# Performance work log

Measured on AMD Instinct MI355X. Metric: run time of the kernel, lower is better.

## Reference

```python
import jax, jax.numpy as jnp
import numpy as np

B, S, D = 4, 2048, 128


def setup_inputs() -> dict:
    key = jax.random.key(0)
    kq, kk, kv = jax.random.split(key, 3)
    query = jax.random.normal(kq, (B, S, D), dtype=jnp.float32)
    key_t = jax.random.normal(kk, (B, S, D), dtype=jnp.float32)
    value = jax.random.normal(kv, (B, S, D), dtype=jnp.float32)
    return {"query": query, "key": key_t, "value": value}


def reference(query, key, value):
    # Raw dot-general attention: contract only the last dim, NO batch dims,
    # so scores have shape [B, Sq, B, Sk] (cross-batch attention).
    scores = jnp.einsum('aqd,bkd->aqbk', query, key)  # [B,S,B,S]
    # softmax over the trailing half of the dims (axes 2 and 3 jointly)
    attn = jax.nn.softmax(scores, axis=(2, 3))
    # Dropout: train=False -> deterministic no-op.
    # Second dot_general contracts trailing (B,Sk) of attn with leading (B,Sk) of value.
    y = jnp.einsum('aqbk,bkd->aqd', attn, value)  # [B,S,D]
    return y
```

## Files before the change

### kernel.cpp

```cpp
#include <hip/hip_runtime.h>
#include <hip/hip_bf16.h>
#include <string.h>

#define NROWS 8192
#define DH    128
#define G     8
#define KPG   (NROWS / G)
#define NIT   (KPG / 64)
#define B32U  (16 * 512)
#define LOG2E 1.44269504088896340736f
#define MSCALED (56.0f * LOG2E)

typedef __attribute__((ext_vector_type(8)))  short    short8;
typedef __attribute__((ext_vector_type(16))) float    floatx16;
typedef __attribute__((ext_vector_type(4)))  unsigned short us4;
typedef __attribute__((ext_vector_type(8)))  _Float16 half8;

#define MFMA_BF32(a, b, c)  __builtin_amdgcn_mfma_f32_32x32x16_bf16((a), (b), (c), 0, 0, 0)
#define MFMA_F16W(a, b, c)  __builtin_amdgcn_mfma_f32_32x32x16_f16((a), (b), (c), 0, 0, 0)

__device__ __forceinline__ unsigned short f32_to_bf16(float f) {
    union { float f; unsigned u; } v; v.f = f;
    unsigned u = v.u + 0x7FFFu + ((v.u >> 16) & 1u);
    return (unsigned short)(u >> 16);
}
__device__ __forceinline__ float bf16_to_f32(unsigned short h) {
    union { unsigned u; float f; } v; v.u = ((unsigned)h) << 16;
    return v.f;
}
__device__ __forceinline__ float fast_exp2(float x) {
    float r; asm("v_exp_f32 %0, %1" : "=v"(r) : "v"(x)); return r;
}
__device__ __forceinline__ void async_ld16(const void* g, void* lds) {
    __builtin_amdgcn_global_load_lds(
        (const __attribute__((address_space(1))) unsigned int*)g,
        (__attribute__((address_space(3))) unsigned int*)lds, 16, 0, 0);
}

__global__ void prep_kernel(const float* __restrict__ K, const float* __restrict__ V,
                            unsigned short* __restrict__ KV) {
    int bid = blockIdx.x;
    if (bid < 128) {
        int B = bid;
        const float* Ksrc = K + (size_t)B * 64 * DH;
        unsigned short* dst = KV + (size_t)(2 * B) * B32U;
#pragma unroll
        for (int j = 0; j < 4; j++) {
            int ch = j * 256 + threadIdx.x;
            int mt = ch >> 9;
            int rem = ch & 511;
            int c = rem >> 6;
            int within = rem & 63;
            int h = within >> 5, l31 = within & 31;
            const float* src = Ksrc + (size_t)(mt * 32 + l31) * DH + c * 16 + h * 8;
            float4 a = *(const float4*)src;
            float4 b = *(const float4*)(src + 4);
            half8 o = {(_Float16)a.x, (_Float16)a.y, (_Float16)a.z, (_Float16)a.w,
                       (_Float16)b.x, (_Float16)b.y, (_Float16)b.z, (_Float16)b.w};
            *(half8*)(dst + (size_t)mt * B32U + c * 512 + within * 8) = o;
        }
        return;
    }
    int B = bid - 128;
    __shared__ unsigned short tile[64][132];
    const float* Vsrc = V + (size_t)B * 64 * DH;
    {
        int row = threadIdx.x >> 2;
        int cb0 = (threadIdx.x & 3) * 32;
#pragma unroll
        for (int j = 0; j < 8; j++) {
            float4 v = *(const float4*)(Vsrc + (size_t)row * DH + cb0 + j * 4);
            tile[row][cb0 + j * 4 + 0] = f32_to_bf16(v.x);
            tile[row][cb0 + j * 4 + 1] = f32_to_bf16(v.y);
            tile[row][cb0 + j * 4 + 2] = f32_to_bf16(v.z);
            tile[row][cb0 + j * 4 + 3] = f32_to_bf16(v.w);
        }
    }
    __syncthreads();
    unsigned short* dstv = KV + (size_t)(2 * B) * B32U + 8 * 512;
#pragma unroll
    for (int j = 0; j < 4; j++) {
        int ch = j * 256 + threadIdx.x;
        int mt = ch >> 9;
        int rem = ch & 511;
        int seg = rem >> 6;
        int within = rem & 63;
        int h = within >> 5, rr = within & 31;
        int t = seg >> 1, sp = seg & 1;
        int d = t * 32 + rr;
        short8 o;
#pragma unroll
        for (int jj = 0; jj < 8; jj++) {
            int p = mt * 32 + sp * 16 + h * 8 + jj;
            int ar = (p & ~12) | ((p & 8) >> 1) | ((p & 4) << 1);
            o[jj] = tile[ar][d];
        }
        *(short8*)(dstv + (size_t)mt * B32U + seg * 512 + within * 8) = o;
    }
}

__launch_bounds__(256, 2)
__global__ void attn_kernel(const float* __restrict__ Q,
                            const unsigned short* __restrict__ KV,
                            unsigned short* __restrict__ Opart,
                            float* __restrict__ lsum) {
    __shared__ __align__(16) unsigned short kbuf[2][16 * 512];

    const int lane = threadIdx.x & 63;
    const int wave = threadIdx.x >> 6;
    const int g    = blockIdx.x & (G - 1);
    const int qt   = blockIdx.x >> 3;
    const int l31  = lane & 31;
    const int h    = lane >> 5;
    const int qrow0 = qt * 128 + wave * 32;

    half8 qf[8];
    {
        const float* qs = Q + (size_t)(qrow0 + l31) * DH + h * 8;
#pragma unroll
        for (int c = 0; c < 8; c++) {
            float4 a = *(const float4*)(qs + c * 16);
            float4 b = *(const float4*)(qs + c * 16 + 4);
            qf[c] = half8{(_Float16)a.x, (_Float16)a.y, (_Float16)a.z, (_Float16)a.w,
                          (_Float16)b.x, (_Float16)b.y, (_Float16)b.z, (_Float16)b.w};
        }
    }

    floatx16 Oacc[4];
#pragma unroll
    for (int t = 0; t < 4; t++)
#pragma unroll
        for (int e = 0; e < 16; e++) Oacc[t][e] = 0.f;
    float lacc = 0.f;

    const unsigned short* pk = KV + (size_t)(g * (KPG / 32)) * B32U + lane * 8;
    const unsigned short* pv = KV + (size_t)(g * (KPG / 32)) * B32U + 8 * 512 + lane * 8;
    auto stage = [&](int buf) {
        unsigned short* dst = kbuf[buf];
#pragma unroll
        for (int j = 0; j < 4; j++) {
            int s = wave + 4 * j;
            int mt = s >> 3, c = s & 7;
            async_ld16(pk + (size_t)(mt * 16 + c) * 512, dst + s * 512);
        }
        pk += 2 * B32U;
    };

    const int fo = lane * 8;

    stage(0);
    for (int it = 0; it < NIT; ++it) {
        __syncthreads();

        short8 vf[16];
#pragma unroll
        for (int s = 0; s < 16; s++) {
            int mt = s >> 3, ss = s & 7;
            vf[s] = *(const short8*)(pv + (size_t)mt * B32U + ss * 512);
        }
        pv += 2 * B32U;

        if (it + 1 < NIT) stage((it + 1) & 1);

        const unsigned short* cb = kbuf[it & 1];

        floatx16 S0, S1;
#pragma unroll
        for (int e = 0; e < 16; e++) { S0[e] = 0.f; S1[e] = 0.f; }
        __builtin_amdgcn_s_setprio(1);
#pragma unroll
        for (int c = 0; c < 8; c++) {
            half8 a0 = *(const half8*)(cb + c * 512 + fo);
            half8 a1 = *(const half8*)(cb + (8 + c) * 512 + fo);
            S0 = MFMA_F16W(a0, qf[c], S0);
            S1 = MFMA_F16W(a1, qf[c], S1);
        }
        __builtin_amdgcn_s_setprio(0);

        short8 bp0[2], bp1[2];
        auto expack = [&](const floatx16& S, short8 (&bp)[2]) {
#pragma unroll
            for (int sp = 0; sp < 2; sp++) {
                union { unsigned u[4]; short8 s8; } pkk;
                float l0 = 0.f, l1 = 0.f;
#pragma unroll
                for (int e = 0; e < 4; e++) {
                    float pa  = fast_exp2(__builtin_fmaf(S[8 * sp + 2 * e],     LOG2E, -MSCALED));
                    float pb2 = fast_exp2(__builtin_fmaf(S[8 * sp + 2 * e + 1], LOG2E, -MSCALED));
                    l0 += pa; l1 += pb2;
                    __hip_bfloat162 c2 = __float22bfloat162_rn(float2{pa, pb2});
                    unsigned u; memcpy(&u, &c2, 4);
                    pkk.u[e] = u;
                }
                lacc += l0 + l1;
                bp[sp] = pkk.s8;
            }
        };
        expack(S0, bp0);
        expack(S1, bp1);

        __builtin_amdgcn_s_setprio(1);
#pragma unroll
        for (int t = 0; t < 4; t++) {
            Oacc[t] = MFMA_BF32(vf[2 * t],     bp0[0], Oacc[t]);
            Oacc[t] = MFMA_BF32(vf[8 + 2 * t], bp1[0], Oacc[t]);
        }
#pragma unroll
        for (int t = 0; t < 4; t++) {
            Oacc[t] = MFMA_BF32(vf[2 * t + 1], bp0[1], Oacc[t]);
            Oacc[t] = MFMA_BF32(vf[9 + 2 * t], bp1[1], Oacc[t]);
        }
        __builtin_amdgcn_s_setprio(0);
    }

    unsigned short* op = Opart + ((size_t)g * NROWS + qrow0 + l31) * DH;
#pragma unroll
    for (int t = 0; t < 4; t++)
#pragma unroll
        for (int rg = 0; rg < 4; rg++) {
            us4 w;
#pragma unroll
            for (int e = 0; e < 4; e++) w[e] = f32_to_bf16(Oacc[t][4 * rg + e]);
            *(us4*)(op + 32 * t + 8 * rg + 4 * h) = w;
        }
    lacc += __shfl_xor(lacc, 32);
    if (h == 0) lsum[(size_t)g * NROWS + qrow0 + l31] = lacc;
}

__global__ void merge_kernel(const unsigned short* __restrict__ Opart,
                             const float* __restrict__ lsum, float* __restrict__ out) {
    int t = blockIdx.x * 256 + threadIdx.x;
    int base = t * 8;
    int q = base >> 7;
    float L = 0.f;
#pragma unroll
    for (int g = 0; g < G; g++) L += lsum[(size_t)g * NROWS + q];
    float acc[8] = {0.f, 0.f, 0.f, 0.f, 0.f, 0.f, 0.f, 0.f};
#pragma unroll
    for (int g = 0; g < G; g++) {
        short8 v = *(const short8*)(Opart + (size_t)g * NROWS * DH + base);
#pragma unroll
        for (int j = 0; j < 8; j++) acc[j] += bf16_to_f32((unsigned short)v[j]);
    }
    float inv = 1.0f / L;
    float4 o0 = {acc[0] * inv, acc[1] * inv, acc[2] * inv, acc[3] * inv};
    float4 o1 = {acc[4] * inv, acc[5] * inv, acc[6] * inv, acc[7] * inv};
    *(float4*)(out + base) = o0;
    *(float4*)(out + base + 4) = o1;
}

extern "C" void kernel_launch(void* const* d_in, const int* in_sizes, int n_in,
                              void* d_out, int out_size, void* d_ws, size_t ws_size,
                              hipStream_t stream) {
    const float* Q = (const float*)d_in[0];
    const float* K = (const float*)d_in[1];
    const float* V = (const float*)d_in[2];
    float* out = (float*)d_out;

    char* ws = (char*)d_ws;
    unsigned short* KV = (unsigned short*)ws;
    char* p = ws + (size_t)(NROWS / 32) * B32U * 2;
    unsigned short* Opart = (unsigned short*)p;
    float* lsum = (float*)(p + (size_t)G * NROWS * DH * sizeof(unsigned short));

    hipLaunchKernelGGL(prep_kernel, dim3(256), dim3(256), 0, stream, K, V, KV);
    hipLaunchKernelGGL(attn_kernel, dim3((NROWS / 128) * G), dim3(256), 0, stream,
                       Q, KV, Opart, lsum);
    hipLaunchKernelGGL(merge_kernel, dim3(NROWS * DH / (256 * 8)), dim3(256), 0, stream,
                       Opart, lsum, out);
}
```

Before: 120.1 us.

## Software-pipeline QK and PV MFMAs with triple-buffered K and LDS-staged V

Restructures the main loop so the QK^T scores for the next tile are computed while the PV MFMAs for the current tile run, interleaving the two MFMA streams. K is triple-buffered in LDS and V is now staged asynchronously into double-buffered LDS instead of being loaded directly from global memory into registers each iteration. This is meant to hide exp latency and global V load latency behind matrix work. In exchange it uses more LDS (five 16 KB buffers), which may reduce occupancy below two blocks per CU, and the prologue/epilogue logic becomes more complex.

```diff
diff --git a/kernel.cpp b/kernel.cpp
--- a/kernel.cpp
+++ b/kernel.cpp
@@ -104,7 +104,8 @@
                             const unsigned short* __restrict__ KV,
                             unsigned short* __restrict__ Opart,
                             float* __restrict__ lsum) {
-    __shared__ __align__(16) unsigned short kbuf[2][16 * 512];
+    __shared__ __align__(16) unsigned short kbuf[3][16 * 512];
+    __shared__ __align__(16) unsigned short vbuf[2][16 * 512];
 
     const int lane = threadIdx.x & 63;
     const int wave = threadIdx.x >> 6;
@@ -133,84 +134,117 @@
         for (int e = 0; e < 16; e++) Oacc[t][e] = 0.f;
     float lacc = 0.f;
 
-    const unsigned short* pk = KV + (size_t)(g * (KPG / 32)) * B32U + lane * 8;
-    const unsigned short* pv = KV + (size_t)(g * (KPG / 32)) * B32U + 8 * 512 + lane * 8;
-    auto stage = [&](int buf) {
-        unsigned short* dst = kbuf[buf];
+    const unsigned short* base = KV + (size_t)(g * (KPG / 32)) * B32U + lane * 8;
+    auto stageK = [&](int tt, int slot) {
+        const unsigned short* src = base + (size_t)(2 * tt) * B32U;
+        unsigned short* dst = kbuf[slot];
 #pragma unroll
         for (int j = 0; j < 4; j++) {
             int s = wave + 4 * j;
             int mt = s >> 3, c = s & 7;
-            async_ld16(pk + (size_t)(mt * 16 + c) * 512, dst + s * 512);
-        }
-        pk += 2 * B32U;
+            async_ld16(src + (size_t)mt * B32U + c * 512, dst + s * 512);
+        }
     };
+    auto stageV = [&](int tt, int slot) {
+        const unsigned short* src = base + (size_t)(2 * tt) * B32U;
+        unsigned short* dst = vbuf[slot];
+#pragma unroll
+        for (int j = 0; j < 4; j++) {
+            int s = wave + 4 * j;
+            int mt = s >> 3, sv = s & 7;
+            async_ld16(src + (size_t)mt * B32U + (8 + sv) * 512, dst + s * 512);
+        }
+    };
 
     const int fo = lane * 8;
 
-    stage(0);
-    for (int it = 0; it < NIT; ++it) {
-        __syncthreads();
-
-        short8 vf[16];
-#pragma unroll
-        for (int s = 0; s < 16; s++) {
-            int mt = s >> 3, ss = s & 7;
-            vf[s] = *(const short8*)(pv + (size_t)mt * B32U + ss * 512);
-        }
-        pv += 2 * B32U;
-
-        if (it + 1 < NIT) stage((it + 1) & 1);
-
-        const unsigned short* cb = kbuf[it & 1];
-
-        floatx16 S0, S1;
-#pragma unroll
-        for (int e = 0; e < 16; e++) { S0[e] = 0.f; S1[e] = 0.f; }
+    stageK(0, 0);
+    stageV(0, 0);
+    stageK(1, 1);
+    __syncthreads();
+
+    floatx16 S0, S1;
+#pragma unroll
+    for (int e = 0; e < 16; e++) { S0[e] = 0.f; S1[e] = 0.f; }
+    {
+        const unsigned short* kb = kbuf[0];
         __builtin_amdgcn_s_setprio(1);
 #pragma unroll
         for (int c = 0; c < 8; c++) {
-            half8 a0 = *(const half8*)(cb + c * 512 + fo);
-            half8 a1 = *(const half8*)(cb + (8 + c) * 512 + fo);
+            half8 a0 = *(const half8*)(kb + c * 512 + fo);
+            half8 a1 = *(const half8*)(kb + (8 + c) * 512 + fo);
             S0 = MFMA_F16W(a0, qf[c], S0);
             S1 = MFMA_F16W(a1, qf[c], S1);
         }
         __builtin_amdgcn_s_setprio(0);
+    }
+
+    int ksl = 1;
+    for (int it = 0; it < NIT; ++it) {
+        int knext = (ksl == 2) ? 0 : ksl + 1;
+        if (it + 2 < NIT) stageK(it + 2, knext);
+        if (it + 1 < NIT) stageV(it + 1, (it + 1) & 1);
 
         short8 bp0[2], bp1[2];
-        auto expack = [&](const floatx16& S, short8 (&bp)[2]) {
+        {
 #pragma unroll
             for (int sp = 0; sp < 2; sp++) {
-                union { unsigned u[4]; short8 s8; } pkk;
+                union { unsigned u[4]; short8 s8; } pk0, pk1;
                 float l0 = 0.f, l1 = 0.f;
 #pragma unroll
                 for (int e = 0; e < 4; e++) {
-                    float pa  = fast_exp2(__builtin_fmaf(S[8 * sp + 2 * e],     LOG2E, -MSCALED));
-                    float pb2 = fast_exp2(__builtin_fmaf(S[8 * sp + 2 * e + 1], LOG2E, -MSCALED));
-                    l0 += pa; l1 += pb2;
-                    __hip_bfloat162 c2 = __float22bfloat162_rn(float2{pa, pb2});
-                    unsigned u; memcpy(&u, &c2, 4);
-                    pkk.u[e] = u;
+                    float a0 = fast_exp2(__builtin_fmaf(S0[8 * sp + 2 * e],     LOG2E, -MSCALED));
+                    float a1 = fast_exp2(__builtin_fmaf(S0[8 * sp + 2 * e + 1], LOG2E, -MSCALED));
+                    float b0 = fast_exp2(__builtin_fmaf(S1[8 * sp + 2 * e],     LOG2E, -MSCALED));
+                    float b1 = fast_exp2(__builtin_fmaf(S1[8 * sp + 2 * e + 1], LOG2E, -MSCALED));
+                    l0 += a0 + a1; l1 += b0 + b1;
+                    __hip_bfloat162 c0 = __float22bfloat162_rn(float2{a0, a1});
+                    __hip_bfloat162 c1 = __float22bfloat162_rn(float2{b0, b1});
+                    unsigned u0, u1;
+                    memcpy(&u0, &c0, 4); memcpy(&u1, &c1, 4);
+                    pk0.u[e] = u0; pk1.u[e] = u1;
                 }
                 lacc += l0 + l1;
-                bp[sp] = pkk.s8;
+                bp0[sp] = pk0.s8;
+                bp1[sp] = pk1.s8;
             }
-        };
-        expack(S0, bp0);
-        expack(S1, bp1);
-
-        __builtin_amdgcn_s_setprio(1);
-#pragma unroll
-        for (int t = 0; t < 4; t++) {
-            Oacc[t] = MFMA_BF32(vf[2 * t],     bp0[0], Oacc[t]);
-            Oacc[t] = MFMA_BF32(vf[8 + 2 * t], bp1[0], Oacc[t]);
-        }
-#pragma unroll
-        for (int t = 0; t < 4; t++) {
-            Oacc[t] = MFMA_BF32(vf[2 * t + 1], bp0[1], Oacc[t]);
-            Oacc[t] = MFMA_BF32(vf[9 + 2 * t], bp1[1], Oacc[t]);
-        }
-        __builtin_amdgcn_s_setprio(0);
+        }
+
+        const unsigned short* vb = vbuf[it & 1];
+        const unsigned short* kb = kbuf[ksl];
+
+        if (it + 1 < NIT) {
+#pragma unroll
+            for (int e = 0; e < 16; e++) { S0[e] = 0.f; S1[e] = 0.f; }
+            __builtin_amdgcn_s_setprio(1);
+#pragma unroll
+            for (int c = 0; c < 8; c++) {
+                half8 a0 = *(const half8*)(kb + c * 512 + fo);
+                half8 a1 = *(const half8*)(kb + (8 + c) * 512 + fo);
+                S0 = MFMA_F16W(a0, qf[c], S0);
+                S1 = MFMA_F16W(a1, qf[c], S1);
+#pragma unroll
+                for (int k = 0; k < 2; k++) {
+                    int p  = 2 * c + k;
+                    int t  = p & 3, sp = (p >> 2) & 1, mt = p >> 3;
+                    short8 vfr = *(const short8*)(vb + (mt * 8 + t * 2 + sp) * 512 + fo);
+                    Oacc[t] = MFMA_BF32(vfr, mt ? bp1[sp] : bp0[sp], Oacc[t]);
+                }
+            }
+            __builtin_amdgcn_s_setprio(0);
+        } else {
+            __builtin_amdgcn_s_setprio(1);
+#pragma unroll
+            for (int p = 0; p < 16; p++) {
+                int t  = p & 3, sp = (p >> 2) & 1, mt = p >> 3;
+                short8 vfr = *(const short8*)(vb + (mt * 8 + t * 2 + sp) * 512 + fo);
+                Oacc[t] = MFMA_BF32(vfr, mt ? bp1[sp] : bp0[sp], Oacc[t]);
+            }
+            __builtin_amdgcn_s_setprio(0);
+        }
+
+        __syncthreads();
+        ksl = knext;
     }
 
     unsigned short* op = Opart + ((size_t)g * NROWS + qrow0 + l31) * DH;
```

Measured after the change: 114.4 us. 4.7% less time.
